# Optimization experiments

Hardware: AMD Instinct MI355X
Metric: run time of the kernel (lower is better)

The kernel has to match this reference:

```python
import jax, jax.numpy as jnp
import numpy as np

B, N, D, H, E, W, OUT = 4, 2048, 128, 4, 32768, 8, 128


def setup_inputs() -> dict:
    key = jax.random.key(0)
    ks = jax.random.split(key, 11)
    s = 0.05  # weight init scale
    return {
        "nodefeatures": jax.random.normal(ks[0], (B, N, D), jnp.float32),
        "node_indices": jax.random.randint(ks[1], (B, 2, E), 0, N),
        "nodeattributes": jax.random.uniform(ks[2], (B, E, W), jnp.float32),
        "wq_w": jax.random.normal(ks[3], (H, D, D), jnp.float32) * s,
        "wq_b": jax.random.normal(ks[4], (H, D), jnp.float32) * s,
        "wk_w": jax.random.normal(ks[5], (H, D, D), jnp.float32) * s,
        "wk_b": jax.random.normal(ks[6], (H, D), jnp.float32) * s,
        "wv_w": jax.random.normal(ks[7], (H, D, D), jnp.float32) * s,
        "wv_b": jax.random.normal(ks[8], (H, D), jnp.float32) * s,
        "out_w": jax.random.normal(ks[9], (OUT, H * D), jnp.float32) * s,
        "out_b": jax.random.normal(ks[10], (OUT,), jnp.float32) * s,
    }


def reference(nodefeatures, node_indices, nodeattributes,
              wq_w, wq_b, wk_w, wk_b, wv_w, wv_b, out_w, out_b):
    b, n, d = nodefeatures.shape
    h = wq_w.shape[0]
    # per-head Linear projections: y = x @ W.T + bias, batched over heads -> [b,h,n,d]
    q = jnp.einsum('bnd,hed->bhne', nodefeatures, wq_w) + wq_b[None, :, None, :]
    k = jnp.einsum('bnd,hed->bhne', nodefeatures, wk_w) + wk_b[None, :, None, :]
    v = jnp.einsum('bnd,hed->bhne', nodefeatures, wv_w) + wv_b[None, :, None, :]

    i = node_indices[:, 0, :]  # [b,E] row indices
    j = node_indices[:, 1, :]  # [b,E] col indices

    # gather q_i, k_j per edge -> [b,h,E,d]; edge score = <q_i,k_j>/sqrt(n)
    qi = jnp.take_along_axis(q, i[:, None, :, None], axis=2)
    kj = jnp.take_along_axis(k, j[:, None, :, None], axis=2)
    wsum = nodeattributes.sum(axis=-1)  # [b,E] (x_edge[:,None]*weights).sum(1)
    # original divides by k.shape[1]**0.5 == sqrt(n)
    edge = (qi * kj).sum(-1) / (n ** 0.5) * wsum[:, None, :]  # [b,h,E]

    # scatter edge scores into zero-initialized dense logits [b,h,n,n]
    bi = jnp.arange(b)[:, None, None]
    hi = jnp.arange(h)[None, :, None]
    scores = jnp.zeros((b, h, n, n), q.dtype).at[bi, hi, i[:, None, :], j[:, None, :]].set(edge)

    attn = jax.nn.softmax(scores, axis=-1)
    o = jnp.einsum('bhnm,bhmd->bhnd', attn, v)
    o = o.transpose(0, 2, 1, 3).reshape(b, n, h * d)  # concat heads on feature dim
    return o @ out_w.T + out_b
```

## Files before the change

### kernel.cpp

```cpp
#include <hip/hip_runtime.h>
#include <hip/hip_bf16.h>
#include <math.h>

constexpr int B_ = 4;
constexpr int N_ = 2048;
constexpr int D_ = 128;
constexpr int H_ = 4;
constexpr int E_ = 32768;
constexpr int W_ = 8;
constexpr int OUT_ = 128;
constexpr int HD_ = H_ * D_;
constexpr int C3_ = 3 * HD_;
constexpr int CAP = 64;
constexpr int M_ = B_ * N_;

typedef __attribute__((ext_vector_type(8))) __bf16 bf16x8;
typedef __attribute__((ext_vector_type(4))) float f32x4;
typedef unsigned int uint32;
typedef unsigned short u16;

__device__ __forceinline__ u16 f2b(float f) {
    __hip_bfloat16 h = __float2bfloat16(f);
    return *(u16*)&h;
}
__device__ __forceinline__ float blo(uint32 u) { return __uint_as_float(u << 16); }
__device__ __forceinline__ float bhi(uint32 u) { return __uint_as_float(u & 0xffff0000u); }

__device__ __forceinline__ void g2l16(const void* g, void* l) {
    __builtin_amdgcn_global_load_lds(
        (const __attribute__((address_space(1))) unsigned int*)(uintptr_t)g,
        (__attribute__((address_space(3))) unsigned int*)(uintptr_t)l,
        16, 0, 0);
}

__global__ __launch_bounds__(256) void prep_kernel(
    const float* __restrict__ X,
    const float* __restrict__ wq, const float* __restrict__ wk, const float* __restrict__ wv,
    const float* __restrict__ bq, const float* __restrict__ bk, const float* __restrict__ bv,
    const float* __restrict__ OW,
    u16* __restrict__ Xbf, u16* __restrict__ Wbf, float* __restrict__ biasf,
    u16* __restrict__ OWbf,
    int* __restrict__ row_count, float* __restrict__ vsum)
{
    const int blk = blockIdx.x;
    if (blk < 512) {
        const int tid = blk * 256 + threadIdx.x;
        const int row = tid >> 4, sub = tid & 15;
        const float4 f0 = *(const float4*)(X + (size_t)row * 128 + sub * 8);
        const float4 f1 = *(const float4*)(X + (size_t)row * 128 + sub * 8 + 4);
        union { u16 u[8]; uint4 v; } pk;
        pk.u[0]=f2b(f0.x); pk.u[1]=f2b(f0.y); pk.u[2]=f2b(f0.z); pk.u[3]=f2b(f0.w);
        pk.u[4]=f2b(f1.x); pk.u[5]=f2b(f1.y); pk.u[6]=f2b(f1.z); pk.u[7]=f2b(f1.w);
        const int ob = row * 256 + ((sub * 16) ^ ((row & 7) << 4));
        *(uint4*)((char*)Xbf + ob) = pk.v;
    } else if (blk < 608) {
        const int c = (blk - 512) * 256 + threadIdx.x;
        const int g = c >> 11, idx = c & 2047;
        const int t3 = g >> 2, h = g & 3;
        const float* Wsrc = (t3 == 0 ? wq : t3 == 1 ? wk : wv) + (size_t)h * 128 * 128;
        const int e = idx >> 4, sub = idx & 15;
        const float4 f0 = *(const float4*)(Wsrc + (size_t)e * 128 + sub * 8);
        const float4 f1 = *(const float4*)(Wsrc + (size_t)e * 128 + sub * 8 + 4);
        union { u16 u[8]; uint4 v; } pk;
        pk.u[0]=f2b(f0.x); pk.u[1]=f2b(f0.y); pk.u[2]=f2b(f0.z); pk.u[3]=f2b(f0.w);
        pk.u[4]=f2b(f1.x); pk.u[5]=f2b(f1.y); pk.u[6]=f2b(f1.z); pk.u[7]=f2b(f1.w);
        const int ob = g * 32768 + e * 256 + ((sub * 16) ^ ((e & 7) << 4));
        *(uint4*)((char*)Wbf + ob) = pk.v;
        if (idx < 128) {
            const float* Bsrc = (t3 == 0 ? bq : t3 == 1 ? bk : bv) + h * 128;
            biasf[g * 128 + idx] = Bsrc[idx];
        }
    } else if (blk < 640) {
        const int tid = (blk - 608) * 256 + threadIdx.x;
        const int c = tid >> 6, sub = tid & 63;
        const float4 f0 = *(const float4*)(OW + (size_t)c * 512 + sub * 8);
        const float4 f1 = *(const float4*)(OW + (size_t)c * 512 + sub * 8 + 4);
        union { u16 u[8]; uint4 v; } pk;
        pk.u[0]=f2b(f0.x); pk.u[1]=f2b(f0.y); pk.u[2]=f2b(f0.z); pk.u[3]=f2b(f0.w);
        pk.u[4]=f2b(f1.x); pk.u[5]=f2b(f1.y); pk.u[6]=f2b(f1.z); pk.u[7]=f2b(f1.w);
        const int ob = c * 1024 + ((sub * 16) ^ ((c & 7) << 4));
        *(uint4*)((char*)OWbf + ob) = pk.v;
    } else {
        const uint4 z = make_uint4(0, 0, 0, 0);
        uint4* rc = (uint4*)row_count;
        #pragma unroll
        for (int q = 0; q < 8; ++q) rc[threadIdx.x + q * 256] = z;
        uint4* vs = (uint4*)vsum;
        #pragma unroll
        for (int q = 0; q < 2; ++q) vs[threadIdx.x + q * 256] = z;
    }
}

__global__ __launch_bounds__(256) void qkv_append(
    const u16* __restrict__ Xbf, const u16* __restrict__ Wbf,
    const float* __restrict__ biasf,
    const int* __restrict__ nidx, const float* __restrict__ attr,
    u16* __restrict__ QKV, float* __restrict__ vsum,
    int* __restrict__ row_count, int2* __restrict__ row_edges)
{
    __shared__ u16 As[128 * 128];
    __shared__ u16 Bs[128 * 128];
    const int t = threadIdx.x;
    const int lane = t & 63, wave = t >> 6;

    if (blockIdx.x >= 768) {
        const int gw0 = (blockIdx.x - 768) * 4 + wave;
        for (int it = 0; it < 16; ++it) {
            const int gw = gw0 + it * 1024;
            const int e0g = gw * 8;
            const int b = e0g / E_;
            const int e0 = e0g % E_;
            float a = attr[((size_t)b * E_ + e0) * W_ + lane];
            a += __shfl_xor(a, 1);
            a += __shfl_xor(a, 2);
            a += __shfl_xor(a, 4);
            if ((lane & 7) == 0) {
                const int sub = lane >> 3;
                const int e = e0 + sub;
                const int i = nidx[b * 2 * E_ + e];
                const int j = nidx[b * 2 * E_ + E_ + e];
                const int pos = atomicAdd(&row_count[b * N_ + i], 1);
                if (pos < CAP)
                    row_edges[(size_t)(b * N_ + i) * CAP + pos] =
                        make_int2(e | (j << 16), __float_as_int(a));
            }
        }
        return;
    }

    const int rb = blockIdx.x & 63;
    const int g  = blockIdx.x >> 6;
    const int wm = wave >> 1, wn = wave & 1;
    const int l15 = lane & 15, l4 = lane >> 4;

    const char* Asrc = (const char*)(Xbf + (size_t)rb * 128 * 128);
    const char* Bsrc = (const char*)(Wbf + (size_t)g  * 128 * 128);
    #pragma unroll
    for (int q = 0; q < 8; ++q) {
        const int o = t * 16 + q * 4096;
        g2l16(Asrc + o, (char*)As + o);
        g2l16(Bsrc + o, (char*)Bs + o);
    }
    __syncthreads();

    f32x4 acc[4][4];
    #pragma unroll
    for (int i = 0; i < 4; ++i)
        #pragma unroll
        for (int j = 0; j < 4; ++j) acc[i][j] = (f32x4){0.f, 0.f, 0.f, 0.f};

    #pragma unroll
    for (int ks = 0; ks < 4; ++ks) {
        const int kb = ks * 64 + l4 * 16;
        bf16x8 a[4], bb[4];
        #pragma unroll
        for (int fm = 0; fm < 4; ++fm) {
            const int row = wm * 64 + fm * 16 + l15;
            a[fm] = *(const bf16x8*)((const char*)As + row * 256 + (kb ^ ((row & 7) << 4)));
        }
        #pragma unroll
        for (int fn = 0; fn < 4; ++fn) {
            const int col = wn * 64 + fn * 16 + l15;
            bb[fn] = *(const bf16x8*)((const char*)Bs + col * 256 + (kb ^ ((col & 7) << 4)));
        }
        #pragma unroll
        for (int fm = 0; fm < 4; ++fm)
            #pragma unroll
            for (int fn = 0; fn < 4; ++fn)
                acc[fm][fn] = __builtin_amdgcn_mfma_f32_16x16x32_bf16(
                    a[fm], bb[fn], acc[fm][fn], 0, 0, 0);
    }

    __syncthreads();

    #pragma unroll
    for (int fm = 0; fm < 4; ++fm)
        #pragma unroll
        for (int fn = 0; fn < 4; ++fn) {
            const int col = wn * 64 + fn * 16 + l15;
            const float bv = biasf[g * 128 + col];
            #pragma unroll
            for (int r = 0; r < 4; ++r) {
                const int row = wm * 64 + fm * 16 + l4 * 4 + r;
                *(u16*)((char*)As + row * 256 + ((col * 2) ^ ((row & 7) << 4))) =
                    f2b(acc[fm][fn][r] + bv);
            }
        }

    if (g >= 8) {
        const int h = g - 8;
        const int b = rb >> 4;
        #pragma unroll
        for (int fn = 0; fn < 4; ++fn) {
            float s = 0.f;
            #pragma unroll
            for (int fm = 0; fm < 4; ++fm)
                #pragma unroll
                for (int r = 0; r < 4; ++r) s += acc[fm][fn][r];
            s += __shfl_xor(s, 16);
            s += __shfl_xor(s, 32);
            if (l4 == 0) {
                const int col = wn * 64 + fn * 16 + l15;
                const float bv = biasf[g * 128 + col];
                atomicAdd(&vsum[(b * H_ + h) * 128 + col], s + 64.f * bv);
            }
        }
    }
    __syncthreads();

    #pragma unroll
    for (int q = 0; q < 8; ++q) {
        const int idx = t + q * 256;
        const int row = idx >> 4, c = idx & 15;
        const uint4 v = *(const uint4*)((char*)As + row * 256 + ((c * 16) ^ ((row & 7) << 4)));
        *(uint4*)(QKV + (size_t)(rb * 128 + row) * C3_ + g * 128 + c * 8) = v;
    }
}

__global__ __launch_bounds__(256) void row_fused(
    const u16* __restrict__ QKV, const float* __restrict__ vsum,
    const int* __restrict__ row_count, const int2* __restrict__ row_edges,
    u16* __restrict__ Obf)
{
    const int t = threadIdx.x;
    const int wave = t >> 6, lane = t & 63;
    const int row = blockIdx.x * 4 + wave;
    const int b = blockIdx.y;
    const int R = b * N_ + row;
    int cnt = row_count[R];
    if (cnt > CAP) cnt = CAP;

    int ej = 0; float ws = 0.f;
    if (lane < cnt) {
        const int2 v = row_edges[(size_t)R * CAP + lane];
        ej = v.x; ws = __int_as_float(v.y);
    }
    const int myj = ej >> 16, mye = ej & 0xFFFF;
    bool win = (lane < cnt);
    for (int p = 0; p < cnt; ++p) {
        const int oj = __shfl(ej, p);
        if (win && (oj >> 16) == myj && (oj & 0xFFFF) > mye) win = false;
    }
    unsigned long long m = __ballot(win);

    const char* base = (const char*)QKV;
    const uint4 qv = *(const uint4*)(base + (size_t)R * 3072 + lane * 16);
    const float q0=blo(qv.x), q1=bhi(qv.x), q2=blo(qv.y), q3=bhi(qv.y),
                q4=blo(qv.z), q5=bhi(qv.z), q6=blo(qv.w), q7=bhi(qv.w);
    const float rs = 0.02209708691207961f;

    float A0=0.f,A1=0.f,A2=0.f,A3=0.f,A4=0.f,A5=0.f,A6=0.f,A7=0.f;
    float B0=0.f,B1=0.f,B2=0.f,B3=0.f,B4=0.f,B5=0.f,B6=0.f,B7=0.f;
    float dsA = 0.f, dsB = 0.f;

#define FETCH(MM, KV1,VV1,W1,KV2,VV2,W2,NN)                                  \
    { int p_ = (int)__ffsll((long long)MM) - 1; MM &= MM - 1;                \
      const int j_ = __shfl(ej, p_) >> 16; W1 = __shfl(ws, p_);              \
      const char* nb_ = base + (size_t)(b * N_ + j_) * 3072;                 \
      KV1 = *(const uint4*)(nb_ + 1024 + lane * 16);                         \
      VV1 = *(const uint4*)(nb_ + 2048 + lane * 16);                         \
      if (MM) {                                                              \
        int q_ = (int)__ffsll((long long)MM) - 1; MM &= MM - 1;              \
        const int j2_ = __shfl(ej, q_) >> 16; W2 = __shfl(ws, q_);           \
        const char* nb2_ = base + (size_t)(b * N_ + j2_) * 3072;             \
        KV2 = *(const uint4*)(nb2_ + 1024 + lane * 16);                      \
        VV2 = *(const uint4*)(nb2_ + 2048 + lane * 16);                      \
        NN = 2;                                                              \
      } else NN = 1; }

#define PROC(kv, vv, wsp, S)                                                 \
    { float s_ = q0*blo(kv.x) + q1*bhi(kv.x) + q2*blo(kv.y) + q3*bhi(kv.y)   \
               + q4*blo(kv.z) + q5*bhi(kv.z) + q6*blo(kv.w) + q7*bhi(kv.w);  \
      s_ += __shfl_xor(s_, 1);                                               \
      s_ += __shfl_xor(s_, 2);                                               \
      s_ += __shfl_xor(s_, 4);                                               \
      s_ += __shfl_xor(s_, 8);                                               \
      const float x_ = expf(s_ * rs * (wsp)) - 1.f;                          \
      ds##S += x_;                                                           \
      S##0 = fmaf(x_, blo(vv.x), S##0); S##1 = fmaf(x_, bhi(vv.x), S##1);    \
      S##2 = fmaf(x_, blo(vv.y), S##2); S##3 = fmaf(x_, bhi(vv.y), S##3);    \
      S##4 = fmaf(x_, blo(vv.z), S##4); S##5 = fmaf(x_, bhi(vv.z), S##5);    \
      S##6 = fmaf(x_, blo(vv.w), S##6); S##7 = fmaf(x_, bhi(vv.w), S##7); }

    if (m) {
        uint4 kv1, vv1, kv2, vv2; float w1, w2; int n1;
        FETCH(m, kv1, vv1, w1, kv2, vv2, w2, n1);
        while (m) {
            uint4 nk1, nv1, nk2, nv2; float nw1, nw2; int n2;
            FETCH(m, nk1, nv1, nw1, nk2, nv2, nw2, n2);
            PROC(kv1, vv1, w1, A);
            if (n1 == 2) PROC(kv2, vv2, w2, B);
            kv1 = nk1; vv1 = nv1; w1 = nw1;
            kv2 = nk2; vv2 = nv2; w2 = nw2; n1 = n2;
        }
        PROC(kv1, vv1, w1, A);
        if (n1 == 2) PROC(kv2, vv2, w2, B);
    }
#undef FETCH
#undef PROC

    const float inv = 1.0f / (2048.0f + dsA + dsB);
    const float* vsp = vsum + (b * H_ + (lane >> 4)) * 128 + (lane & 15) * 8;
    const float4 vs0 = *(const float4*)vsp;
    const float4 vs1 = *(const float4*)(vsp + 4);
    union { u16 u[8]; uint4 v; } o;
    o.u[0]=f2b((vs0.x+A0+B0)*inv); o.u[1]=f2b((vs0.y+A1+B1)*inv);
    o.u[2]=f2b((vs0.z+A2+B2)*inv); o.u[3]=f2b((vs0.w+A3+B3)*inv);
    o.u[4]=f2b((vs1.x+A4+B4)*inv); o.u[5]=f2b((vs1.y+A5+B5)*inv);
    o.u[6]=f2b((vs1.z+A6+B6)*inv); o.u[7]=f2b((vs1.w+A7+B7)*inv);
    const int ob = ((lane >> 4) << 8) + (((lane & 15) * 16) ^ ((R & 7) << 4));
    *(uint4*)((char*)Obf + (size_t)R * 1024 + ob) = o.v;
}

__global__ __launch_bounds__(256) void out_mfma(
    const u16* __restrict__ Obf, const u16* __restrict__ OWbf,
    const float* __restrict__ bo, float* __restrict__ Out)
{
    __shared__ u16 As[32 * 128];
    __shared__ u16 Bs[128 * 128];
    const int rb = blockIdx.x;
    const int t = threadIdx.x;
    const int lane = t & 63, wave = t >> 6;
    const int wm = wave >> 1, wn = wave & 1;
    const int l15 = lane & 15, l4 = lane >> 4;

    f32x4 acc[4];
    #pragma unroll
    for (int j = 0; j < 4; ++j) acc[j] = (f32x4){0.f, 0.f, 0.f, 0.f};

    for (int kc = 0; kc < 4; ++kc) {
        #pragma unroll
        for (int q = 0; q < 2; ++q) {
            const int o = t * 16 + q * 4096;
            const int arow = o >> 8, ob = o & 255;
            g2l16((const char*)Obf + (size_t)(rb * 32 + arow) * 1024 + kc * 256 + ob,
                  (char*)As + o);
        }
        #pragma unroll
        for (int q = 0; q < 8; ++q) {
            const int o = t * 16 + q * 4096;
            const int c = o >> 8, ob = o & 255;
            g2l16((const char*)OWbf + (size_t)c * 1024 + kc * 256 + ob,
                  (char*)Bs + o);
        }
        __syncthreads();
        #pragma unroll
        for (int ks = 0; ks < 4; ++ks) {
            const int kb = ks * 64 + l4 * 16;
            bf16x8 a0, bb[4];
            {
                const int row = wm * 16 + l15;
                a0 = *(const bf16x8*)((const char*)As + row * 256 + (kb ^ ((row & 7) << 4)));
            }
            #pragma unroll
            for (int fn = 0; fn < 4; ++fn) {
                const int col = wn * 64 + fn * 16 + l15;
                bb[fn] = *(const bf16x8*)((const char*)Bs + col * 256 + (kb ^ ((col & 7) << 4)));
            }
            #pragma unroll
            for (int fn = 0; fn < 4; ++fn)
                acc[fn] = __builtin_amdgcn_mfma_f32_16x16x32_bf16(
                    a0, bb[fn], acc[fn], 0, 0, 0);
        }
        __syncthreads();
    }

    #pragma unroll
    for (int fn = 0; fn < 4; ++fn) {
        const int col = wn * 64 + fn * 16 + l15;
        const float bv = bo[col];
        #pragma unroll
        for (int r = 0; r < 4; ++r) {
            const int row = rb * 32 + wm * 16 + l4 * 4 + r;
            Out[(size_t)row * OUT_ + col] = acc[fn][r] + bv;
        }
    }
}

extern "C" void kernel_launch(void* const* d_in, const int* in_sizes, int n_in,
                              void* d_out, int out_size, void* d_ws, size_t ws_size,
                              hipStream_t stream)
{
    const float* x     = (const float*)d_in[0];
    const int*   nidx  = (const int*)  d_in[1];
    const float* attr  = (const float*)d_in[2];
    const float* wq_w  = (const float*)d_in[3];
    const float* wq_b  = (const float*)d_in[4];
    const float* wk_w  = (const float*)d_in[5];
    const float* wk_b  = (const float*)d_in[6];
    const float* wv_w  = (const float*)d_in[7];
    const float* wv_b  = (const float*)d_in[8];
    const float* out_w = (const float*)d_in[9];
    const float* out_b = (const float*)d_in[10];
    float* out = (float*)d_out;

    char* ws = (char*)d_ws;
    size_t off = 0;
    auto alloc = [&](size_t bytes) -> char* {
        char* p = ws + off;
        off += (bytes + 255) & ~(size_t)255;
        return p;
    };
    u16*  Xbf  = (u16*)alloc((size_t)M_ * D_ * 2);
    u16*  Wbf  = (u16*)alloc((size_t)12 * D_ * D_ * 2);
    float* biasf = (float*)alloc((size_t)12 * D_ * 4);
    u16*  QKV  = (u16*)alloc((size_t)M_ * C3_ * 2);
    u16*  OWbf = (u16*)alloc((size_t)OUT_ * HD_ * 2);
    u16*  Obf  = (u16*)alloc((size_t)M_ * HD_ * 2);
    float* vsum = (float*)alloc((size_t)B_ * H_ * D_ * 4);
    int*  row_count = (int*)alloc((size_t)B_ * N_ * 4);
    int2* row_edges = (int2*)alloc((size_t)B_ * N_ * CAP * 8);

    prep_kernel<<<641, 256, 0, stream>>>(
        x, wq_w, wk_w, wv_w, wq_b, wk_b, wv_b, out_w,
        Xbf, Wbf, biasf, OWbf, row_count, vsum);
    qkv_append<<<1024, 256, 0, stream>>>(
        Xbf, Wbf, biasf, nidx, attr, QKV, vsum, row_count, row_edges);
    row_fused<<<dim3(N_ / 4, B_), 256, 0, stream>>>(
        QKV, vsum, row_count, row_edges, Obf);
    out_mfma<<<M_ / 32, 256, 0, stream>>>(Obf, OWbf, out_b, out);
}
```

Before: 79.18 us.

## Read GEMM operands directly from global, widen edge-append grid, split rows over two waves

The QKV GEMM now reads A and B fragments straight from global memory in plain row-major bf16 instead of staging them through swizzled LDS. This drops the LDS load, the barrier and 64KB of shared memory per block, so occupancy can rise. The edge-append path becomes one iteration per wave across 4096 extra blocks instead of a 16-iteration loop. row_fused splits each row's edges between two waves and combines the partial sums through shared memory, doubling the grid to expose more parallelism at the cost of a sync and extra q/mask work.

```diff
diff --git a/kernel.cpp b/kernel.cpp
--- a/kernel.cpp
+++ b/kernel.cpp
@@ -45,27 +45,23 @@
     const int blk = blockIdx.x;
     if (blk < 512) {
         const int tid = blk * 256 + threadIdx.x;
-        const int row = tid >> 4, sub = tid & 15;
-        const float4 f0 = *(const float4*)(X + (size_t)row * 128 + sub * 8);
-        const float4 f1 = *(const float4*)(X + (size_t)row * 128 + sub * 8 + 4);
+        const float4 f0 = *(const float4*)(X + (size_t)tid * 8);
+        const float4 f1 = *(const float4*)(X + (size_t)tid * 8 + 4);
         union { u16 u[8]; uint4 v; } pk;
         pk.u[0]=f2b(f0.x); pk.u[1]=f2b(f0.y); pk.u[2]=f2b(f0.z); pk.u[3]=f2b(f0.w);
         pk.u[4]=f2b(f1.x); pk.u[5]=f2b(f1.y); pk.u[6]=f2b(f1.z); pk.u[7]=f2b(f1.w);
-        const int ob = row * 256 + ((sub * 16) ^ ((row & 7) << 4));
-        *(uint4*)((char*)Xbf + ob) = pk.v;
+        *(uint4*)((char*)Xbf + (size_t)tid * 16) = pk.v;
     } else if (blk < 608) {
         const int c = (blk - 512) * 256 + threadIdx.x;
         const int g = c >> 11, idx = c & 2047;
         const int t3 = g >> 2, h = g & 3;
         const float* Wsrc = (t3 == 0 ? wq : t3 == 1 ? wk : wv) + (size_t)h * 128 * 128;
-        const int e = idx >> 4, sub = idx & 15;
-        const float4 f0 = *(const float4*)(Wsrc + (size_t)e * 128 + sub * 8);
-        const float4 f1 = *(const float4*)(Wsrc + (size_t)e * 128 + sub * 8 + 4);
+        const float4 f0 = *(const float4*)(Wsrc + (size_t)idx * 8);
+        const float4 f1 = *(const float4*)(Wsrc + (size_t)idx * 8 + 4);
         union { u16 u[8]; uint4 v; } pk;
         pk.u[0]=f2b(f0.x); pk.u[1]=f2b(f0.y); pk.u[2]=f2b(f0.z); pk.u[3]=f2b(f0.w);
         pk.u[4]=f2b(f1.x); pk.u[5]=f2b(f1.y); pk.u[6]=f2b(f1.z); pk.u[7]=f2b(f1.w);
-        const int ob = g * 32768 + e * 256 + ((sub * 16) ^ ((e & 7) << 4));
-        *(uint4*)((char*)Wbf + ob) = pk.v;
+        *(uint4*)((char*)Wbf + (size_t)c * 16) = pk.v;
         if (idx < 128) {
             const float* Bsrc = (t3 == 0 ? bq : t3 == 1 ? bk : bv) + h * 128;
             biasf[g * 128 + idx] = Bsrc[idx];
@@ -98,32 +94,28 @@
     u16* __restrict__ QKV, float* __restrict__ vsum,
     int* __restrict__ row_count, int2* __restrict__ row_edges)
 {
-    __shared__ u16 As[128 * 128];
-    __shared__ u16 Bs[128 * 128];
+    __shared__ u16 Cs[128 * 128];
     const int t = threadIdx.x;
     const int lane = t & 63, wave = t >> 6;
 
     if (blockIdx.x >= 768) {
-        const int gw0 = (blockIdx.x - 768) * 4 + wave;
-        for (int it = 0; it < 16; ++it) {
-            const int gw = gw0 + it * 1024;
-            const int e0g = gw * 8;
-            const int b = e0g / E_;
-            const int e0 = e0g % E_;
-            float a = attr[((size_t)b * E_ + e0) * W_ + lane];
-            a += __shfl_xor(a, 1);
-            a += __shfl_xor(a, 2);
-            a += __shfl_xor(a, 4);
-            if ((lane & 7) == 0) {
-                const int sub = lane >> 3;
-                const int e = e0 + sub;
-                const int i = nidx[b * 2 * E_ + e];
-                const int j = nidx[b * 2 * E_ + E_ + e];
-                const int pos = atomicAdd(&row_count[b * N_ + i], 1);
-                if (pos < CAP)
-                    row_edges[(size_t)(b * N_ + i) * CAP + pos] =
-                        make_int2(e | (j << 16), __float_as_int(a));
-            }
+        const int gw = (blockIdx.x - 768) * 4 + wave;
+        const int e0g = gw * 8;
+        const int b = e0g / E_;
+        const int e0 = e0g % E_;
+        float a = attr[((size_t)b * E_ + e0) * W_ + lane];
+        a += __shfl_xor(a, 1);
+        a += __shfl_xor(a, 2);
+        a += __shfl_xor(a, 4);
+        if ((lane & 7) == 0) {
+            const int sub = lane >> 3;
+            const int e = e0 + sub;
+            const int i = nidx[b * 2 * E_ + e];
+            const int j = nidx[b * 2 * E_ + E_ + e];
+            const int pos = atomicAdd(&row_count[b * N_ + i], 1);
+            if (pos < CAP)
+                row_edges[(size_t)(b * N_ + i) * CAP + pos] =
+                    make_int2(e | (j << 16), __float_as_int(a));
         }
         return;
     }
@@ -133,15 +125,8 @@
     const int wm = wave >> 1, wn = wave & 1;
     const int l15 = lane & 15, l4 = lane >> 4;
 
-    const char* Asrc = (const char*)(Xbf + (size_t)rb * 128 * 128);
-    const char* Bsrc = (const char*)(Wbf + (size_t)g  * 128 * 128);
-    #pragma unroll
-    for (int q = 0; q < 8; ++q) {
-        const int o = t * 16 + q * 4096;
-        g2l16(Asrc + o, (char*)As + o);
-        g2l16(Bsrc + o, (char*)Bs + o);
-    }
-    __syncthreads();
+    const u16* Abase = Xbf + (size_t)(rb * 128) * 128;
+    const u16* Bbase = Wbf + (size_t)(g  * 128) * 128;
 
     f32x4 acc[4][4];
     #pragma unroll
@@ -151,18 +136,14 @@
 
     #pragma unroll
     for (int ks = 0; ks < 4; ++ks) {
-        const int kb = ks * 64 + l4 * 16;
+        const int ko = ks * 32 + l4 * 8;
         bf16x8 a[4], bb[4];
         #pragma unroll
-        for (int fm = 0; fm < 4; ++fm) {
-            const int row = wm * 64 + fm * 16 + l15;
-            a[fm] = *(const bf16x8*)((const char*)As + row * 256 + (kb ^ ((row & 7) << 4)));
-        }
-        #pragma unroll
-        for (int fn = 0; fn < 4; ++fn) {
-            const int col = wn * 64 + fn * 16 + l15;
-            bb[fn] = *(const bf16x8*)((const char*)Bs + col * 256 + (kb ^ ((col & 7) << 4)));
-        }
+        for (int fm = 0; fm < 4; ++fm)
+            a[fm] = *(const bf16x8*)(Abase + (wm * 64 + fm * 16 + l15) * 128 + ko);
+        #pragma unroll
+        for (int fn = 0; fn < 4; ++fn)
+            bb[fn] = *(const bf16x8*)(Bbase + (wn * 64 + fn * 16 + l15) * 128 + ko);
         #pragma unroll
         for (int fm = 0; fm < 4; ++fm)
             #pragma unroll
@@ -170,8 +151,6 @@
                 acc[fm][fn] = __builtin_amdgcn_mfma_f32_16x16x32_bf16(
                     a[fm], bb[fn], acc[fm][fn], 0, 0, 0);
     }
-
-    __syncthreads();
 
     #pragma unroll
     for (int fm = 0; fm < 4; ++fm)
@@ -182,7 +161,7 @@
             #pragma unroll
             for (int r = 0; r < 4; ++r) {
                 const int row = wm * 64 + fm * 16 + l4 * 4 + r;
-                *(u16*)((char*)As + row * 256 + ((col * 2) ^ ((row & 7) << 4))) =
+                *(u16*)((char*)Cs + row * 256 + ((col * 2) ^ ((row & 7) << 4))) =
                     f2b(acc[fm][fn][r] + bv);
             }
         }
@@ -212,7 +191,7 @@
     for (int q = 0; q < 8; ++q) {
         const int idx = t + q * 256;
         const int row = idx >> 4, c = idx & 15;
-        const uint4 v = *(const uint4*)((char*)As + row * 256 + ((c * 16) ^ ((row & 7) << 4)));
+        const uint4 v = *(const uint4*)((char*)Cs + row * 256 + ((c * 16) ^ ((row & 7) << 4)));
         *(uint4*)(QKV + (size_t)(rb * 128 + row) * C3_ + g * 128 + c * 8) = v;
     }
 }
@@ -224,7 +203,8 @@
 {
     const int t = threadIdx.x;
     const int wave = t >> 6, lane = t & 63;
-    const int row = blockIdx.x * 4 + wave;
+    const int rid = wave >> 1, half = wave & 1;
+    const int row = blockIdx.x * 2 + rid;
     const int b = blockIdx.y;
     const int R = b * N_ + row;
     int cnt = row_count[R];
@@ -241,7 +221,9 @@
         const int oj = __shfl(ej, p);
         if (win && (oj >> 16) == myj && (oj & 0xFFFF) > mye) win = false;
     }
-    unsigned long long m = __ballot(win);
+    const unsigned long long wmask = __ballot(win);
+    const int pos = (int)__popcll(wmask & ((1ull << lane) - 1ull));
+    unsigned long long m = __ballot(win && ((pos & 1) == half));
 
     const char* base = (const char*)QKV;
     const uint4 qv = *(const uint4*)(base + (size_t)R * 3072 + lane * 16);
@@ -299,17 +281,30 @@
 #undef FETCH
 #undef PROC
 
-    const float inv = 1.0f / (2048.0f + dsA + dsB);
-    const float* vsp = vsum + (b * H_ + (lane >> 4)) * 128 + (lane & 15) * 8;
-    const float4 vs0 = *(const float4*)vsp;
-    const float4 vs1 = *(const float4*)(vsp + 4);
-    union { u16 u[8]; uint4 v; } o;
-    o.u[0]=f2b((vs0.x+A0+B0)*inv); o.u[1]=f2b((vs0.y+A1+B1)*inv);
-    o.u[2]=f2b((vs0.z+A2+B2)*inv); o.u[3]=f2b((vs0.w+A3+B3)*inv);
-    o.u[4]=f2b((vs1.x+A4+B4)*inv); o.u[5]=f2b((vs1.y+A5+B5)*inv);
-    o.u[6]=f2b((vs1.z+A6+B6)*inv); o.u[7]=f2b((vs1.w+A7+B7)*inv);
-    const int ob = ((lane >> 4) << 8) + (((lane & 15) * 16) ^ ((R & 7) << 4));
-    *(uint4*)((char*)Obf + (size_t)R * 1024 + ob) = o.v;
+    __shared__ float part[2][64][9];
+    if (half == 1) {
+        float* p = part[rid][lane];
+        p[0]=A0+B0; p[1]=A1+B1; p[2]=A2+B2; p[3]=A3+B3;
+        p[4]=A4+B4; p[5]=A5+B5; p[6]=A6+B6; p[7]=A7+B7;
+        p[8]=dsA+dsB;
+    }
+    __syncthreads();
+    if (half == 0) {
+        const float* p = part[rid][lane];
+        const float o0=A0+B0+p[0], o1=A1+B1+p[1], o2=A2+B2+p[2], o3=A3+B3+p[3];
+        const float o4=A4+B4+p[4], o5=A5+B5+p[5], o6=A6+B6+p[6], o7=A7+B7+p[7];
+        const float inv = 1.0f / (2048.0f + dsA + dsB + p[8]);
+        const float* vsp = vsum + (b * H_ + (lane >> 4)) * 128 + (lane & 15) * 8;
+        const float4 vs0 = *(const float4*)vsp;
+        const float4 vs1 = *(const float4*)(vsp + 4);
+        union { u16 u[8]; uint4 v; } o;
+        o.u[0]=f2b((vs0.x+o0)*inv); o.u[1]=f2b((vs0.y+o1)*inv);
+        o.u[2]=f2b((vs0.z+o2)*inv); o.u[3]=f2b((vs0.w+o3)*inv);
+        o.u[4]=f2b((vs1.x+o4)*inv); o.u[5]=f2b((vs1.y+o5)*inv);
+        o.u[6]=f2b((vs1.z+o6)*inv); o.u[7]=f2b((vs1.w+o7)*inv);
+        const int ob = ((lane >> 4) << 8) + (((lane & 15) * 16) ^ ((R & 7) << 4));
+        *(uint4*)((char*)Obf + (size_t)R * 1024 + ob) = o.v;
+    }
 }
 
 __global__ __launch_bounds__(256) void out_mfma(
@@ -414,9 +409,9 @@
     prep_kernel<<<641, 256, 0, stream>>>(
         x, wq_w, wk_w, wv_w, wq_b, wk_b, wv_b, out_w,
         Xbf, Wbf, biasf, OWbf, row_count, vsum);
-    qkv_append<<<1024, 256, 0, stream>>>(
+    qkv_append<<<768 + 4096, 256, 0, stream>>>(
         Xbf, Wbf, biasf, nidx, attr, QKV, vsum, row_count, row_edges);
-    row_fused<<<dim3(N_ / 4, B_), 256, 0, stream>>>(
+    row_fused<<<dim3(N_ / 2, B_), 256, 0, stream>>>(
         QKV, vsum, row_count, row_edges, Obf);
     out_mfma<<<M_ / 32, 256, 0, stream>>>(Obf, OWbf, out_b, out);
 }
```

Measured after the change: 81.15 us. +2.5%, slower.
